# Kernel tuning notes

Hardware: AMD Instinct MI355X
Metric: run time of the kernel (lower is better)

The kernel has to match this reference:

```python
import jax, jax.numpy as jnp
import numpy as np
from jax import lax

N_HEADS = 8
KERNEL = 3
PAD = 1
D_MODEL = 512

def setup_inputs() -> dict:
    key = jax.random.key(0)
    k1, k2, k3 = jax.random.split(key, 3)
    x = jax.random.normal(k1, (64, 1024, D_MODEL), dtype=jnp.float32)
    weight = jax.random.normal(k2, (N_HEADS, 1, KERNEL), dtype=jnp.float32)
    fc_w = jax.random.normal(k3, (D_MODEL, D_MODEL), dtype=jnp.float32) * (1.0 / np.sqrt(D_MODEL))
    return {"x": x, "weight": weight, "fc_w": fc_w}

def reference(x, weight, fc_w):
    bs, gs, d_model = x.shape
    # weight_softmax=True: normalize kernel taps per head
    w = jax.nn.softmax(weight, axis=-1)  # [H, 1, K]
    # view(-1, n_heads, d_model): channels = heads, spatial axis = d_model
    x2 = x.reshape(-1, N_HEADS, d_model)  # [bs*gs/H, H, d_model]
    out = lax.conv_general_dilated(
        x2, w,
        window_strides=(1,),
        padding=[(PAD, PAD)],
        feature_group_count=N_HEADS,
        dimension_numbers=("NCH", "OIH", "NCH"),
    )  # depthwise conv along d_model
    out = out.reshape(bs, gs, d_model)
    # nn.Linear without bias: y = out @ fc_w.T
    return jnp.einsum("bgd,ed->bge", out, fc_w)
```

## Files before the change

kernel.cpp:

```cpp
#include <hip/hip_runtime.h>

typedef __attribute__((ext_vector_type(8))) __bf16  bf16x8;
typedef __attribute__((ext_vector_type(8))) short   short8;
typedef __attribute__((ext_vector_type(4))) float   f32x4;

#define DM   512
#define BM   256
#define BN   256
#define BK   64
#define NNT  2
#define NKT  8
#define TILEB 32768

__device__ __forceinline__ short f2bf(float f) {
  union { float f; unsigned u; } v; v.f = f;
  unsigned r = v.u + 0x7fffu + ((v.u >> 16) & 1u);
  return (short)(r >> 16);
}

__device__ __forceinline__ int swz(int r, int cbyte) {
  return (r * 128 + cbyte) ^ ((r & 7) << 4);
}

__global__ void build_g_kernel(const float* __restrict__ w,
                               const float* __restrict__ fcw,
                               short* __restrict__ Gt) {
  int idx = blockIdx.x * 256 + threadIdx.x;
  int h = idx >> 18;
  int e = (idx >> 9) & 511;
  int d = idx & 511;
  float w0 = w[h*3+0], w1 = w[h*3+1], w2 = w[h*3+2];
  float mx = fmaxf(w0, fmaxf(w1, w2));
  float e0 = __expf(w0-mx), e1 = __expf(w1-mx), e2 = __expf(w2-mx);
  float inv = 1.0f / (e0 + e1 + e2);
  const float* row = fcw + e * DM;
  float acc = e1 * inv * row[d];
  if (d < DM-1) acc += e0 * inv * row[d+1];
  if (d > 0)    acc += e2 * inv * row[d-1];
  int nt = e >> 8, r = e & 255;
  int kt = d >> 6, c = d & 63;
  char* tile = (char*)Gt + (size_t)((h * NNT + nt) * NKT + kt) * TILEB;
  *(short*)(tile + swz(r, c * 2)) = f2bf(acc);
}

__global__ __launch_bounds__(512, 2) void gemm_kernel(const float* __restrict__ x,
                                                      const short* __restrict__ Gt,
                                                      float* __restrict__ out) {
  int bid = blockIdx.x;
  int h  = bid & 7;
  int nt = (bid >> 3) & 1;
  int mt = bid >> 4;
  int tid  = threadIdx.x;
  int lane = tid & 63;
  int wid  = tid >> 6;
  int wr = wid >> 2, wc = wid & 3;

  __shared__ short Alds[2][BM * BK];
  __shared__ short Blds[2][BN * BK];

  const char* Bsrc0 = (const char*)Gt + (size_t)(h * NNT + nt) * NKT * TILEB;
  const float* Abase = x + (size_t)(h + 8 * (size_t)mt * BM) * DM;

  float4 ap[8];

  auto loadA = [&](int kt) {
    #pragma unroll
    for (int p = 0; p < 4; ++p) {
      int r = (tid >> 3) + 64 * p;
      const float* xr = Abase + (size_t)r * 8 * DM + kt * BK + (tid & 7) * 8;
      ap[2*p]   = *(const float4*)xr;
      ap[2*p+1] = *(const float4*)(xr + 4);
    }
  };
  auto stageB = [&](int kt, int buf) {
    const char* src = Bsrc0 + kt * TILEB;
    char* dst = (char*)Blds[buf];
    #pragma unroll
    for (int p = 0; p < 4; ++p)
      __builtin_amdgcn_global_load_lds((const void*)(src + p * 8192 + tid * 16),
                                       (void*)(dst + p * 8192 + wid * 1024), 16, 0, 0);
  };
  auto writeA = [&](int buf) {
    char* dst = (char*)Alds[buf];
    #pragma unroll
    for (int p = 0; p < 4; ++p) {
      int r = (tid >> 3) + 64 * p;
      short8 sv;
      sv[0]=f2bf(ap[2*p].x);   sv[1]=f2bf(ap[2*p].y);
      sv[2]=f2bf(ap[2*p].z);   sv[3]=f2bf(ap[2*p].w);
      sv[4]=f2bf(ap[2*p+1].x); sv[5]=f2bf(ap[2*p+1].y);
      sv[6]=f2bf(ap[2*p+1].z); sv[7]=f2bf(ap[2*p+1].w);
      *(short8*)(dst + swz(r, (tid & 7) * 16)) = sv;
    }
  };

  f32x4 acc[8][4] = {};

  loadA(0);
  stageB(0, 0);
  writeA(0);
  __syncthreads();

  for (int kt = 0; kt < NKT; ++kt) {
    int cur = kt & 1, nxt = cur ^ 1;

    if (kt + 1 < NKT) {
      loadA(kt + 1);
      stageB(kt + 1, nxt);
    }

    const char* Ap = (const char*)Alds[cur];
    const char* Bp = (const char*)Blds[cur];
    #pragma unroll
    for (int ks = 0; ks < 2; ++ks) {
      bf16x8 af[8], bfr[4];
      #pragma unroll
      for (int m = 0; m < 8; ++m)
        af[m] = *(const bf16x8*)(Ap + swz(wr*128 + m*16 + (lane & 15),
                                          ks*64 + (lane >> 4) * 16));
      #pragma unroll
      for (int n = 0; n < 4; ++n)
        bfr[n] = *(const bf16x8*)(Bp + swz(wc*64 + n*16 + (lane & 15),
                                           ks*64 + (lane >> 4) * 16));
      #pragma unroll
      for (int m = 0; m < 8; ++m)
        #pragma unroll
        for (int n = 0; n < 4; ++n)
          acc[m][n] = __builtin_amdgcn_mfma_f32_16x16x32_bf16(af[m], bfr[n], acc[m][n], 0, 0, 0);
    }

    if (kt + 1 < NKT) writeA(nxt);
    __syncthreads();
  }

  int e0 = nt * BN + wc * 64 + (lane & 15);
  #pragma unroll
  for (int m = 0; m < 8; ++m) {
    int tq = mt * BM + wr * 128 + m * 16 + ((lane >> 4) << 2);
    #pragma unroll
    for (int j = 0; j < 4; ++j) {
      int R = h + 8 * (tq + j);
      float* orow = out + (size_t)R * DM + e0;
      #pragma unroll
      for (int n = 0; n < 4; ++n)
        orow[n * 16] = acc[m][n][j];
    }
  }
}

extern "C" void kernel_launch(void* const* d_in, const int* in_sizes, int n_in,
                              void* d_out, int out_size, void* d_ws, size_t ws_size,
                              hipStream_t stream) {
  const float* x   = (const float*)d_in[0];
  const float* w   = (const float*)d_in[1];
  const float* fcw = (const float*)d_in[2];
  float* out = (float*)d_out;
  short* Gt  = (short*)d_ws;

  hipLaunchKernelGGL(build_g_kernel, dim3((8 * DM * DM) / 256), dim3(256), 0, stream,
                     w, fcw, Gt);
  hipLaunchKernelGGL(gemm_kernel, dim3(8 * 32 * NNT), dim3(512), 0, stream,
                     x, Gt, out);
}
```

Before: 79.74 us.

## Vectorize weight-fold kernel and interleave LDS reads with MFMA in phased GEMM loop

The build kernel now has each thread compute eight consecutive bf16 outputs using float4 loads and a single 16-byte store, cutting thread count and store traffic. The GEMM main loop is split into four phases that alternate LDS fragment reads with 16-MFMA batches. Workgroup barriers, explicit lgkmcnt waits and setprio raise around the MFMAs are added, and global prefetches are spread across the phases. This aims to overlap memory and math across waves, at the cost of extra barriers per K-tile.

```diff
diff --git a/kernel.cpp b/kernel.cpp
--- a/kernel.cpp
+++ b/kernel.cpp
@@ -26,21 +26,31 @@
                                const float* __restrict__ fcw,
                                short* __restrict__ Gt) {
   int idx = blockIdx.x * 256 + threadIdx.x;
-  int h = idx >> 18;
-  int e = (idx >> 9) & 511;
-  int d = idx & 511;
+  int h  = idx >> 15;
+  int t  = idx & 32767;
+  int e  = t >> 6;
+  int d0 = (t & 63) << 3;
   float w0 = w[h*3+0], w1 = w[h*3+1], w2 = w[h*3+2];
   float mx = fmaxf(w0, fmaxf(w1, w2));
   float e0 = __expf(w0-mx), e1 = __expf(w1-mx), e2 = __expf(w2-mx);
   float inv = 1.0f / (e0 + e1 + e2);
+  float w0n = e0*inv, w1n = e1*inv, w2n = e2*inv;
   const float* row = fcw + e * DM;
-  float acc = e1 * inv * row[d];
-  if (d < DM-1) acc += e0 * inv * row[d+1];
-  if (d > 0)    acc += e2 * inv * row[d-1];
+  float v[10];
+  v[0] = (d0 > 0) ? row[d0-1] : 0.0f;
+  float4 a = *(const float4*)(row + d0);
+  float4 b = *(const float4*)(row + d0 + 4);
+  v[1]=a.x; v[2]=a.y; v[3]=a.z; v[4]=a.w;
+  v[5]=b.x; v[6]=b.y; v[7]=b.z; v[8]=b.w;
+  v[9] = (d0 + 8 < DM) ? row[d0+8] : 0.0f;
+  short8 sv;
+  #pragma unroll
+  for (int j = 0; j < 8; ++j)
+    sv[j] = f2bf(w1n*v[j+1] + w0n*v[j+2] + w2n*v[j]);
   int nt = e >> 8, r = e & 255;
-  int kt = d >> 6, c = d & 63;
+  int kt = d0 >> 6, c = d0 & 63;
   char* tile = (char*)Gt + (size_t)((h * NNT + nt) * NKT + kt) * TILEB;
-  *(short*)(tile + swz(r, c * 2)) = f2bf(acc);
+  *(short8*)(tile + swz(r, c * 2)) = sv;
 }
 
 __global__ __launch_bounds__(512, 2) void gemm_kernel(const float* __restrict__ x,
@@ -96,40 +106,64 @@
 
   f32x4 acc[8][4] = {};
 
+  auto rdA = [&](bf16x8* af, const char* Ap, int mh, int ks) {
+    #pragma unroll
+    for (int m = 0; m < 4; ++m)
+      af[m] = *(const bf16x8*)(Ap + swz(wr*128 + (mh*4 + m)*16 + (lane & 15),
+                                        ks*64 + (lane >> 4) * 16));
+  };
+  auto rdB = [&](bf16x8* bfr, const char* Bp, int ks) {
+    #pragma unroll
+    for (int n = 0; n < 4; ++n)
+      bfr[n] = *(const bf16x8*)(Bp + swz(wc*64 + n*16 + (lane & 15),
+                                         ks*64 + (lane >> 4) * 16));
+  };
+  auto mma16 = [&](bf16x8* af, bf16x8* bfr, int mh) {
+    #pragma unroll
+    for (int m = 0; m < 4; ++m)
+      #pragma unroll
+      for (int n = 0; n < 4; ++n)
+        acc[mh*4 + m][n] = __builtin_amdgcn_mfma_f32_16x16x32_bf16(af[m], bfr[n],
+                                                                   acc[mh*4 + m][n], 0, 0, 0);
+  };
+
+#define SBAR()  do { __builtin_amdgcn_s_barrier(); __builtin_amdgcn_sched_barrier(0); } while (0)
+#define LGKM0() do { asm volatile("s_waitcnt lgkmcnt(0)" ::: "memory"); \
+                     __builtin_amdgcn_sched_barrier(0); } while (0)
+
   loadA(0);
   stageB(0, 0);
   writeA(0);
   __syncthreads();
 
   for (int kt = 0; kt < NKT; ++kt) {
-    int cur = kt & 1, nxt = cur ^ 1;
-
-    if (kt + 1 < NKT) {
-      loadA(kt + 1);
-      stageB(kt + 1, nxt);
-    }
-
-    const char* Ap = (const char*)Alds[cur];
-    const char* Bp = (const char*)Blds[cur];
-    #pragma unroll
-    for (int ks = 0; ks < 2; ++ks) {
-      bf16x8 af[8], bfr[4];
-      #pragma unroll
-      for (int m = 0; m < 8; ++m)
-        af[m] = *(const bf16x8*)(Ap + swz(wr*128 + m*16 + (lane & 15),
-                                          ks*64 + (lane >> 4) * 16));
-      #pragma unroll
-      for (int n = 0; n < 4; ++n)
-        bfr[n] = *(const bf16x8*)(Bp + swz(wc*64 + n*16 + (lane & 15),
-                                           ks*64 + (lane >> 4) * 16));
-      #pragma unroll
-      for (int m = 0; m < 8; ++m)
-        #pragma unroll
-        for (int n = 0; n < 4; ++n)
-          acc[m][n] = __builtin_amdgcn_mfma_f32_16x16x32_bf16(af[m], bfr[n], acc[m][n], 0, 0, 0);
-    }
-
-    if (kt + 1 < NKT) writeA(nxt);
+    int nxt = (kt & 1) ^ 1;
+    const char* Ap = (const char*)Alds[kt & 1];
+    const char* Bp = (const char*)Blds[kt & 1];
+    bool pre = (kt + 1 < NKT);
+    bf16x8 af[4], bf0[4];
+
+    rdB(bf0, Bp, 0); rdA(af, Ap, 0, 0);
+    if (pre) loadA(kt + 1);
+    SBAR(); LGKM0();
+    __builtin_amdgcn_s_setprio(1); mma16(af, bf0, 0); __builtin_amdgcn_s_setprio(0);
+    SBAR();
+
+    rdA(af, Ap, 1, 0);
+    if (pre) stageB(kt + 1, nxt);
+    SBAR(); LGKM0();
+    __builtin_amdgcn_s_setprio(1); mma16(af, bf0, 1); __builtin_amdgcn_s_setprio(0);
+    SBAR();
+
+    rdB(bf0, Bp, 1); rdA(af, Ap, 0, 1);
+    SBAR(); LGKM0();
+    __builtin_amdgcn_s_setprio(1); mma16(af, bf0, 0); __builtin_amdgcn_s_setprio(0);
+    SBAR();
+
+    rdA(af, Ap, 1, 1);
+    SBAR(); LGKM0();
+    __builtin_amdgcn_s_setprio(1); mma16(af, bf0, 1); __builtin_amdgcn_s_setprio(0);
+    if (pre) writeA(nxt);
     __syncthreads();
   }
 
@@ -146,6 +180,8 @@
         orow[n * 16] = acc[m][n][j];
     }
   }
+#undef SBAR
+#undef LGKM0
 }
 
 extern "C" void kernel_launch(void* const* d_in, const int* in_sizes, int n_in,
@@ -157,7 +193,7 @@
   float* out = (float*)d_out;
   short* Gt  = (short*)d_ws;
 
-  hipLaunchKernelGGL(build_g_kernel, dim3((8 * DM * DM) / 256), dim3(256), 0, stream,
+  hipLaunchKernelGGL(build_g_kernel, dim3((8 * DM * DM / 8) / 256), dim3(256), 0, stream,
                      w, fcw, Gt);
   hipLaunchKernelGGL(gemm_kernel, dim3(8 * 32 * NNT), dim3(512), 0, stream,
                      x, Gt, out);
```

New measurement: 88.79 us. 1.11x slower.

## Prefetch A two tiles ahead with manual vmcnt waits; vectorize G build

Applied to the files above, without the earlier changes.

The GEMM main loop is fully unrolled and uses two register buffers for the fp32 A tiles, so global loads run two k-tiles ahead. Each tile boundary uses an explicit s_waitcnt vmcnt(8) with sched barriers in place of __syncthreads, so outstanding prefetches do not have to drain. The build_g kernel now has each thread produce 8 bf16 outputs with float4 loads and a single 16-byte store. The cost is higher register pressure under launch_bounds(512,2), and the hand-set vmcnt counts must match the real number of issued loads for the results to be correct.

```diff
diff --git a/kernel.cpp b/kernel.cpp
--- a/kernel.cpp
+++ b/kernel.cpp
@@ -26,21 +26,31 @@
                                const float* __restrict__ fcw,
                                short* __restrict__ Gt) {
   int idx = blockIdx.x * 256 + threadIdx.x;
-  int h = idx >> 18;
-  int e = (idx >> 9) & 511;
-  int d = idx & 511;
+  int h  = idx >> 15;
+  int t  = idx & 32767;
+  int e  = t >> 6;
+  int d0 = (t & 63) << 3;
   float w0 = w[h*3+0], w1 = w[h*3+1], w2 = w[h*3+2];
   float mx = fmaxf(w0, fmaxf(w1, w2));
   float e0 = __expf(w0-mx), e1 = __expf(w1-mx), e2 = __expf(w2-mx);
   float inv = 1.0f / (e0 + e1 + e2);
+  float w0n = e0*inv, w1n = e1*inv, w2n = e2*inv;
   const float* row = fcw + e * DM;
-  float acc = e1 * inv * row[d];
-  if (d < DM-1) acc += e0 * inv * row[d+1];
-  if (d > 0)    acc += e2 * inv * row[d-1];
+  float v[10];
+  v[0] = (d0 > 0) ? row[d0-1] : 0.0f;
+  float4 a = *(const float4*)(row + d0);
+  float4 b = *(const float4*)(row + d0 + 4);
+  v[1]=a.x; v[2]=a.y; v[3]=a.z; v[4]=a.w;
+  v[5]=b.x; v[6]=b.y; v[7]=b.z; v[8]=b.w;
+  v[9] = (d0 + 8 < DM) ? row[d0+8] : 0.0f;
+  short8 sv;
+  #pragma unroll
+  for (int j = 0; j < 8; ++j)
+    sv[j] = f2bf(w1n*v[j+1] + w0n*v[j+2] + w2n*v[j]);
   int nt = e >> 8, r = e & 255;
-  int kt = d >> 6, c = d & 63;
+  int kt = d0 >> 6, c = d0 & 63;
   char* tile = (char*)Gt + (size_t)((h * NNT + nt) * NKT + kt) * TILEB;
-  *(short*)(tile + swz(r, c * 2)) = f2bf(acc);
+  *(short8*)(tile + swz(r, c * 2)) = sv;
 }
 
 __global__ __launch_bounds__(512, 2) void gemm_kernel(const float* __restrict__ x,
@@ -61,9 +71,9 @@
   const char* Bsrc0 = (const char*)Gt + (size_t)(h * NNT + nt) * NKT * TILEB;
   const float* Abase = x + (size_t)(h + 8 * (size_t)mt * BM) * DM;
 
-  float4 ap[8];
+  float4 ap0[8], ap1[8];
 
-  auto loadA = [&](int kt) {
+  auto loadA = [&](int kt, float4 (&ap)[8]) {
     #pragma unroll
     for (int p = 0; p < 4; ++p) {
       int r = (tid >> 3) + 64 * p;
@@ -80,7 +90,7 @@
       __builtin_amdgcn_global_load_lds((const void*)(src + p * 8192 + tid * 16),
                                        (void*)(dst + p * 8192 + wid * 1024), 16, 0, 0);
   };
-  auto writeA = [&](int buf) {
+  auto writeA = [&](float4 (&ap)[8], int buf) {
     char* dst = (char*)Alds[buf];
     #pragma unroll
     for (int p = 0; p < 4; ++p) {
@@ -96,19 +106,7 @@
 
   f32x4 acc[8][4] = {};
 
-  loadA(0);
-  stageB(0, 0);
-  writeA(0);
-  __syncthreads();
-
-  for (int kt = 0; kt < NKT; ++kt) {
-    int cur = kt & 1, nxt = cur ^ 1;
-
-    if (kt + 1 < NKT) {
-      loadA(kt + 1);
-      stageB(kt + 1, nxt);
-    }
-
+  auto computeTile = [&](int cur) {
     const char* Ap = (const char*)Alds[cur];
     const char* Bp = (const char*)Blds[cur];
     #pragma unroll
@@ -128,10 +126,43 @@
         for (int n = 0; n < 4; ++n)
           acc[m][n] = __builtin_amdgcn_mfma_f32_16x16x32_bf16(af[m], bfr[n], acc[m][n], 0, 0, 0);
     }
+  };
 
-    if (kt + 1 < NKT) writeA(nxt);
-    __syncthreads();
-  }
+#define BOUNDARY(VMSTR)                                                   \
+  do {                                                                    \
+    asm volatile(VMSTR ::: "memory");                                     \
+    __builtin_amdgcn_sched_barrier(0);                                    \
+    __builtin_amdgcn_s_barrier();                                         \
+    __builtin_amdgcn_sched_barrier(0);                                    \
+  } while (0)
+
+#define GITER(T, APC, APN, VMSTR)                                         \
+  do {                                                                    \
+    if ((T) + 1 < NKT) stageB((T) + 1, ((T) + 1) & 1);                    \
+    if ((T) + 2 < NKT) loadA((T) + 2, APC);                               \
+    __builtin_amdgcn_sched_barrier(0);                                    \
+    computeTile((T) & 1);                                                 \
+    if ((T) + 1 < NKT) writeA(APN, ((T) + 1) & 1);                        \
+    BOUNDARY(VMSTR);                                                      \
+  } while (0)
+
+  loadA(0, ap0);
+  stageB(0, 0);
+  loadA(1, ap1);
+  writeA(ap0, 0);
+  BOUNDARY("s_waitcnt vmcnt(8) lgkmcnt(0)");
+
+  GITER(0, ap0, ap1, "s_waitcnt vmcnt(8) lgkmcnt(0)");
+  GITER(1, ap1, ap0, "s_waitcnt vmcnt(8) lgkmcnt(0)");
+  GITER(2, ap0, ap1, "s_waitcnt vmcnt(8) lgkmcnt(0)");
+  GITER(3, ap1, ap0, "s_waitcnt vmcnt(8) lgkmcnt(0)");
+  GITER(4, ap0, ap1, "s_waitcnt vmcnt(8) lgkmcnt(0)");
+  GITER(5, ap1, ap0, "s_waitcnt vmcnt(8) lgkmcnt(0)");
+  GITER(6, ap0, ap1, "s_waitcnt vmcnt(0) lgkmcnt(0)");
+  computeTile(1);
+
+#undef GITER
+#undef BOUNDARY
 
   int e0 = nt * BN + wc * 64 + (lane & 15);
   #pragma unroll
@@ -157,7 +188,7 @@
   float* out = (float*)d_out;
   short* Gt  = (short*)d_ws;
 
-  hipLaunchKernelGGL(build_g_kernel, dim3((8 * DM * DM) / 256), dim3(256), 0, stream,
+  hipLaunchKernelGGL(build_g_kernel, dim3((8 * DM * DM / 8) / 256), dim3(256), 0, stream,
                      w, fcw, Gt);
   hipLaunchKernelGGL(gemm_kernel, dim3(8 * 32 * NNT), dim3(512), 0, stream,
                      x, Gt, out);
```

Result: slower. 85.24 us (+6.9%).

## Process both N tiles per block and vectorize G-matrix construction

Applied to the files above, without the earlier changes.

Each GEMM block now computes both 256-wide output column tiles in sequence, and the second tile's prologue is overlapped with the first tile's output store. This halves the grid to 256 blocks and may improve reuse of the x rows in cache, though the A tile is still reloaded from global memory per tile. The build kernel now has each thread produce 8 consecutive bf16 outputs with vector loads and a 16-byte store instead of scalar work. The risk is lower parallelism: 256 blocks of 512 threads may underfill the GPU and leave compute units idle.

```diff
diff --git a/kernel.cpp b/kernel.cpp
--- a/kernel.cpp
+++ b/kernel.cpp
@@ -26,30 +26,39 @@
                                const float* __restrict__ fcw,
                                short* __restrict__ Gt) {
   int idx = blockIdx.x * 256 + threadIdx.x;
-  int h = idx >> 18;
-  int e = (idx >> 9) & 511;
-  int d = idx & 511;
+  int h  = idx >> 15;
+  int t  = idx & 32767;
+  int e  = t >> 6;
+  int d0 = (t & 63) << 3;
   float w0 = w[h*3+0], w1 = w[h*3+1], w2 = w[h*3+2];
   float mx = fmaxf(w0, fmaxf(w1, w2));
   float e0 = __expf(w0-mx), e1 = __expf(w1-mx), e2 = __expf(w2-mx);
   float inv = 1.0f / (e0 + e1 + e2);
+  float w0n = e0*inv, w1n = e1*inv, w2n = e2*inv;
   const float* row = fcw + e * DM;
-  float acc = e1 * inv * row[d];
-  if (d < DM-1) acc += e0 * inv * row[d+1];
-  if (d > 0)    acc += e2 * inv * row[d-1];
+  float v[10];
+  v[0] = (d0 > 0) ? row[d0-1] : 0.0f;
+  float4 a = *(const float4*)(row + d0);
+  float4 b = *(const float4*)(row + d0 + 4);
+  v[1]=a.x; v[2]=a.y; v[3]=a.z; v[4]=a.w;
+  v[5]=b.x; v[6]=b.y; v[7]=b.z; v[8]=b.w;
+  v[9] = (d0 + 8 < DM) ? row[d0+8] : 0.0f;
+  short8 sv;
+  #pragma unroll
+  for (int j = 0; j < 8; ++j)
+    sv[j] = f2bf(w1n*v[j+1] + w0n*v[j+2] + w2n*v[j]);
   int nt = e >> 8, r = e & 255;
-  int kt = d >> 6, c = d & 63;
+  int kt = d0 >> 6, c = d0 & 63;
   char* tile = (char*)Gt + (size_t)((h * NNT + nt) * NKT + kt) * TILEB;
-  *(short*)(tile + swz(r, c * 2)) = f2bf(acc);
+  *(short8*)(tile + swz(r, c * 2)) = sv;
 }
 
 __global__ __launch_bounds__(512, 2) void gemm_kernel(const float* __restrict__ x,
                                                       const short* __restrict__ Gt,
                                                       float* __restrict__ out) {
   int bid = blockIdx.x;
-  int h  = bid & 7;
-  int nt = (bid >> 3) & 1;
-  int mt = bid >> 4;
+  int h   = bid & 7;
+  int mt  = bid >> 3;
   int tid  = threadIdx.x;
   int lane = tid & 63;
   int wid  = tid >> 6;
@@ -58,7 +67,7 @@
   __shared__ short Alds[2][BM * BK];
   __shared__ short Blds[2][BN * BK];
 
-  const char* Bsrc0 = (const char*)Gt + (size_t)(h * NNT + nt) * NKT * TILEB;
+  const char* BsrcH = (const char*)Gt + (size_t)(h * NNT) * NKT * TILEB;
   const float* Abase = x + (size_t)(h + 8 * (size_t)mt * BM) * DM;
 
   float4 ap[8];
@@ -72,8 +81,8 @@
       ap[2*p+1] = *(const float4*)(xr + 4);
     }
   };
-  auto stageB = [&](int kt, int buf) {
-    const char* src = Bsrc0 + kt * TILEB;
+  auto stageB = [&](int rep, int kt, int buf) {
+    const char* src = BsrcH + (size_t)rep * NKT * TILEB + kt * TILEB;
     char* dst = (char*)Blds[buf];
     #pragma unroll
     for (int p = 0; p < 4; ++p)
@@ -94,21 +103,13 @@
     }
   };
 
-  f32x4 acc[8][4] = {};
+  f32x4 acc[8][4];
+  #pragma unroll
+  for (int m = 0; m < 8; ++m)
+    #pragma unroll
+    for (int n = 0; n < 4; ++n) acc[m][n] = (f32x4){0.f, 0.f, 0.f, 0.f};
 
-  loadA(0);
-  stageB(0, 0);
-  writeA(0);
-  __syncthreads();
-
-  for (int kt = 0; kt < NKT; ++kt) {
-    int cur = kt & 1, nxt = cur ^ 1;
-
-    if (kt + 1 < NKT) {
-      loadA(kt + 1);
-      stageB(kt + 1, nxt);
-    }
-
+  auto computeTile = [&](int cur) {
     const char* Ap = (const char*)Alds[cur];
     const char* Bp = (const char*)Blds[cur];
     #pragma unroll
@@ -128,24 +129,52 @@
         for (int n = 0; n < 4; ++n)
           acc[m][n] = __builtin_amdgcn_mfma_f32_16x16x32_bf16(af[m], bfr[n], acc[m][n], 0, 0, 0);
     }
+  };
 
-    if (kt + 1 < NKT) writeA(nxt);
+  auto prologue = [&](int rep) {
+    loadA(0);
+    stageB(rep, 0, 0);
+    writeA(0);
     __syncthreads();
-  }
+  };
+  auto kloop = [&](int rep) {
+    for (int kt = 0; kt < NKT; ++kt) {
+      int cur = kt & 1, nxt = cur ^ 1;
+      if (kt + 1 < NKT) {
+        loadA(kt + 1);
+        stageB(rep, kt + 1, nxt);
+      }
+      computeTile(cur);
+      if (kt + 1 < NKT) writeA(nxt);
+      __syncthreads();
+    }
+  };
+  auto storeC = [&](int rep) {
+    int e0 = rep * BN + wc * 64 + (lane & 15);
+    #pragma unroll
+    for (int m = 0; m < 8; ++m) {
+      int tq = mt * BM + wr * 128 + m * 16 + ((lane >> 4) << 2);
+      #pragma unroll
+      for (int j = 0; j < 4; ++j) {
+        int R = h + 8 * (tq + j);
+        float* orow = out + (size_t)R * DM + e0;
+        #pragma unroll
+        for (int n = 0; n < 4; ++n)
+          orow[n * 16] = acc[m][n][j];
+      }
+    }
+  };
 
-  int e0 = nt * BN + wc * 64 + (lane & 15);
+  prologue(0);
+  kloop(0);
+  prologue(1);
+  storeC(0);
   #pragma unroll
-  for (int m = 0; m < 8; ++m) {
-    int tq = mt * BM + wr * 128 + m * 16 + ((lane >> 4) << 2);
+  for (int m = 0; m < 8; ++m)
     #pragma unroll
-    for (int j = 0; j < 4; ++j) {
-      int R = h + 8 * (tq + j);
-      float* orow = out + (size_t)R * DM + e0;
-      #pragma unroll
-      for (int n = 0; n < 4; ++n)
-        orow[n * 16] = acc[m][n][j];
-    }
-  }
+    for (int n = 0; n < 4; ++n) acc[m][n] = (f32x4){0.f, 0.f, 0.f, 0.f};
+  kloop(1);
+  storeC(1);
 }
 
 extern "C" void kernel_launch(void* const* d_in, const int* in_sizes, int n_in,
@@ -157,8 +186,8 @@
   float* out = (float*)d_out;
   short* Gt  = (short*)d_ws;
 
-  hipLaunchKernelGGL(build_g_kernel, dim3((8 * DM * DM) / 256), dim3(256), 0, stream,
+  hipLaunchKernelGGL(build_g_kernel, dim3((8 * DM * DM / 8) / 256), dim3(256), 0, stream,
                      w, fcw, Gt);
-  hipLaunchKernelGGL(gemm_kernel, dim3(8 * 32 * NNT), dim3(512), 0, stream,
+  hipLaunchKernelGGL(gemm_kernel, dim3(8 * 32), dim3(512), 0, stream,
                      x, Gt, out);
 }
```

Measured after the change: 97.58 us. +22.4%, slower.
